# Performance work log

Hardware: AMD Instinct MI355X
Metric: run time of the kernel (lower is better)

## Reference

```python
import jax, jax.numpy as jnp
import numpy as np

B, S, D = 2, 2048, 2048
H = 16
Q_LORA, KV_LORA = 1536, 512
D_NOPE, D_ROPE, D_V = 128, 64, 128
D_QK = D_NOPE + D_ROPE  # 192
EPS = 1e-6


def rmsnorm(x, w):
    return x * jax.lax.rsqrt(jnp.mean(x * x, axis=-1, keepdims=True) + EPS) * w


def apply_rope(x, freqs_cis):
    # x: (B, S, h, D_ROPE); freqs_cis: (S, D_ROPE//2, 2) = (cos, sin)
    # DeepSeek pairs consecutive elements (2i, 2i+1) as complex re/im.
    b, s, h, d = x.shape
    xp = x.reshape(b, s, h, d // 2, 2)
    re, im = xp[..., 0], xp[..., 1]
    cos = freqs_cis[None, :, None, :, 0]
    sin = freqs_cis[None, :, None, :, 1]
    out_re = re * cos - im * sin
    out_im = re * sin + im * cos
    return jnp.stack([out_re, out_im], axis=-1).reshape(b, s, h, d)


def setup_inputs() -> dict:
    key = jax.random.key(0)
    ks = jax.random.split(key, 8)
    sd = 0.02
    x = jax.random.normal(ks[0], (B, S, D), dtype=jnp.float32)
    # RoPE table over the rope head dim
    inv_freq = 1.0 / (10000.0 ** (np.arange(0, D_ROPE, 2, dtype=np.float32) / D_ROPE))
    t = np.arange(S, dtype=np.float32)
    f = np.outer(t, inv_freq)  # (S, 32)
    freqs_cis = jnp.asarray(np.stack([np.cos(f), np.sin(f)], axis=-1), dtype=jnp.float32)
    return {
        "x": x,
        "start_pos": 0,
        "freqs_cis": freqs_cis,
        "wq_a": jax.random.normal(ks[1], (Q_LORA, D), dtype=jnp.float32) * sd,
        "q_norm_w": jnp.ones((Q_LORA,), dtype=jnp.float32),
        "wq_b": jax.random.normal(ks[2], (H * D_QK, Q_LORA), dtype=jnp.float32) * sd,
        "wkv_a": jax.random.normal(ks[3], (KV_LORA + D_ROPE, D), dtype=jnp.float32) * sd,
        "kv_norm_w": jnp.ones((KV_LORA,), dtype=jnp.float32),
        "wkv_b": jax.random.normal(ks[4], (H * (D_NOPE + D_V), KV_LORA), dtype=jnp.float32) * sd,
        "wo": jax.random.normal(ks[5], (D, H * D_V), dtype=jnp.float32) * sd,
    }


def reference(x, start_pos, freqs_cis, wq_a, q_norm_w, wq_b, wkv_a, kv_norm_w, wkv_b, wo):
    bsz, seqlen, _ = x.shape
    softmax_scale = D_QK ** (-0.5)

    # --- queries: low-rank down-proj, RMSNorm, up-proj ---
    q = rmsnorm(x @ wq_a.T, q_norm_w) @ wq_b.T          # (B,S,H*D_QK)
    q = q.reshape(bsz, seqlen, H, D_QK)
    q_nope, q_pe = q[..., :D_NOPE], q[..., D_NOPE:]
    q_pe = apply_rope(q_pe, freqs_cis)
    q = jnp.concatenate([q_nope, q_pe], axis=-1)         # (B,S,H,192)

    # --- keys/values: compressed latent + shared rope key ---
    kv = x @ wkv_a.T                                     # (B,S,KV_LORA+D_ROPE)
    kv_c, k_pe = kv[..., :KV_LORA], kv[..., KV_LORA:]
    k_pe = apply_rope(k_pe[:, :, None, :], freqs_cis)    # (B,S,1,64)
    kvb = rmsnorm(kv_c, kv_norm_w) @ wkv_b.T             # (B,S,H*(D_NOPE+D_V))
    kvb = kvb.reshape(bsz, seqlen, H, D_NOPE + D_V)
    k_nope, v = kvb[..., :D_NOPE], kvb[..., D_NOPE:]
    k = jnp.concatenate([k_nope, jnp.broadcast_to(k_pe, (bsz, seqlen, H, D_ROPE))], axis=-1)

    # --- causal attention (FA2 with attention_mask=None) ---
    scores = jnp.einsum("bqhd,bkhd->bhqk", q, k) * softmax_scale
    causal = jnp.tril(jnp.ones((seqlen, seqlen), dtype=bool))
    scores = jnp.where(causal[None, None], scores, jnp.finfo(scores.dtype).min)
    attn = jax.nn.softmax(scores, axis=-1)
    out = jnp.einsum("bhqk,bkhd->bqhd", attn, v)         # (B,S,H,D_V)
    # (v padding to qk_head_dim then slicing [..., :D_V] is a no-op)
    return out.reshape(bsz, seqlen, H * D_V) @ wo.T
```

## Files before the change

### kernel.cpp

```cpp
#include <hip/hip_runtime.h>
#include <math.h>

typedef short short8 __attribute__((ext_vector_type(8)));
typedef float float4v __attribute__((ext_vector_type(4)));
#define AS1 __attribute__((address_space(1)))
#define AS3 __attribute__((address_space(3)))

__device__ __forceinline__ float b2f(ushort u) {
    unsigned v = ((unsigned)u) << 16; float f; __builtin_memcpy(&f, &v, 4); return f;
}
__device__ __forceinline__ ushort f2b(float f) {
    unsigned v; __builtin_memcpy(&v, &f, 4);
    unsigned r = (v + 0x7fffu + ((v >> 16) & 1u)) >> 16;
    return (ushort)r;
}

__global__ void cvt_pad(const float* __restrict__ src, ushort* __restrict__ dst,
                        int src_rows, int cols, int total4) {
    int i = blockIdx.x * 256 + threadIdx.x;
    if (i >= total4) return;
    size_t e = (size_t)i * 4;
    int r = (int)(e / (size_t)cols);
    ushort4 o;
    if (r < src_rows) {
        float4 v = *(const float4*)(src + e);
        o.x = f2b(v.x); o.y = f2b(v.y); o.z = f2b(v.z); o.w = f2b(v.w);
    } else {
        o.x = 0; o.y = 0; o.z = 0; o.w = 0;
    }
    *(ushort4*)(dst + e) = o;
}

__global__ __launch_bounds__(256)
void gemm_bt(const ushort* __restrict__ A, const ushort* __restrict__ B,
             void* __restrict__ Cv, int K, int lda, int ldb, int ldc, int mode,
             ushort* __restrict__ Kf, ushort* __restrict__ Vtp) {
    __shared__ ushort sA[128 * 32];
    __shared__ ushort sB[128 * 32];
    const int tid = threadIdx.x;
    const int wave = tid >> 6, lane = tid & 63;
    const int bm = blockIdx.y * 128, bn = blockIdx.x * 128;
    const int wm = (wave >> 1) * 64, wn = (wave & 1) * 64;
    const int lq = lane & 15, quad = lane >> 4;
    float4v acc[4][4] = {};

    const int srow = wave * 32 + (lane >> 2);
    const int skc = (lane & 3) * 8;
    const ushort* Ag = A + (size_t)(bm + srow) * lda + skc;
    const ushort* Bg = B + (size_t)(bn + srow) * ldb + skc;
    ushort* sAw = sA + (wave * 32) * 32;
    ushort* sBw = sB + (wave * 32) * 32;

    for (int k0 = 0; k0 < K; k0 += 32) {
        __builtin_amdgcn_global_load_lds((const AS1 void*)(Ag + k0), (AS3 void*)sAw, 16, 0, 0);
        __builtin_amdgcn_global_load_lds((const AS1 void*)(Ag + (size_t)16 * lda + k0),
                                         (AS3 void*)(sAw + 16 * 32), 16, 0, 0);
        __builtin_amdgcn_global_load_lds((const AS1 void*)(Bg + k0), (AS3 void*)sBw, 16, 0, 0);
        __builtin_amdgcn_global_load_lds((const AS1 void*)(Bg + (size_t)16 * ldb + k0),
                                         (AS3 void*)(sBw + 16 * 32), 16, 0, 0);
        __syncthreads();
        short8 af[4], bfr[4];
#pragma unroll
        for (int i = 0; i < 4; ++i) {
            af[i]  = *(const short8*)(sA + (wm + i * 16 + lq) * 32 + quad * 8);
            bfr[i] = *(const short8*)(sB + (wn + i * 16 + lq) * 32 + quad * 8);
        }
#pragma unroll
        for (int i = 0; i < 4; ++i)
#pragma unroll
            for (int j = 0; j < 4; ++j)
                acc[i][j] = __builtin_amdgcn_mfma_f32_16x16x32_bf16(af[i], bfr[j], acc[i][j], 0, 0, 0);
        __syncthreads();
    }
#pragma unroll
    for (int i = 0; i < 4; ++i) {
        int row0 = bm + wm + i * 16 + quad * 4;
#pragma unroll
        for (int j = 0; j < 4; ++j) {
            int col = bn + wn + j * 16 + lq;
            if (mode == 0) {
                ushort* C = (ushort*)Cv;
#pragma unroll
                for (int r = 0; r < 4; ++r)
                    C[(size_t)(row0 + r) * ldc + col] = f2b(acc[i][j][r]);
            } else if (mode == 1) {
                float* C = (float*)Cv;
#pragma unroll
                for (int r = 0; r < 4; ++r)
                    C[(size_t)(row0 + r) * ldc + col] = acc[i][j][r];
            } else {
                int h = col >> 8, c = col & 255;
                int bh = ((row0 >> 11) << 4) + h;
                if (c < 128) {
#pragma unroll
                    for (int r = 0; r < 4; ++r) {
                        int s = (row0 + r) & 2047;
                        Kf[((size_t)bh * 2048 + s) * 200 + c] = f2b(acc[i][j][r]);
                    }
                } else {
                    int d = c - 128;
                    int kt = (row0 & 2047) >> 6, kv = row0 & 63;
                    ushort4 o;
                    o.x = f2b(acc[i][j][0]); o.y = f2b(acc[i][j][1]);
                    o.z = f2b(acc[i][j][2]); o.w = f2b(acc[i][j][3]);
                    *(ushort4*)(Vtp + (((size_t)bh * 32 + kt) * 128 + d) * 72 + kv) = o;
                }
            }
        }
    }
}

__global__ void rmsnorm_inplace(ushort* __restrict__ d, const float* __restrict__ w,
                                int cols, int ld) {
    int row = blockIdx.x, tid = threadIdx.x;
    ushort* p = d + (size_t)row * ld;
    float ss = 0.f;
    for (int i = tid; i < cols; i += 256) { float v = b2f(p[i]); ss += v * v; }
#pragma unroll
    for (int off = 32; off >= 1; off >>= 1) ss += __shfl_xor(ss, off);
    __shared__ float red[4];
    if ((tid & 63) == 0) red[tid >> 6] = ss;
    __syncthreads();
    float tot = red[0] + red[1] + red[2] + red[3];
    float rs = rsqrtf(tot / (float)cols + 1e-6f);
    for (int i = tid; i < cols; i += 256) p[i] = f2b(b2f(p[i]) * rs * w[i]);
}

__global__ void kvnorm_rope(const ushort* __restrict__ kvraw, const float* __restrict__ w,
                            const float* __restrict__ freqs, ushort* __restrict__ kvc,
                            ushort* __restrict__ kpe, int ld) {
    int row = blockIdx.x, tid = threadIdx.x;
    int s = row & 2047;
    const ushort* p = kvraw + (size_t)row * ld;
    float v0 = b2f(p[tid]), v1 = b2f(p[tid + 256]);
    float ss = v0 * v0 + v1 * v1;
#pragma unroll
    for (int off = 32; off >= 1; off >>= 1) ss += __shfl_xor(ss, off);
    __shared__ float red[4];
    if ((tid & 63) == 0) red[tid >> 6] = ss;
    __syncthreads();
    float tot = red[0] + red[1] + red[2] + red[3];
    float rs = rsqrtf(tot / 512.f + 1e-6f);
    kvc[(size_t)row * 512 + tid] = f2b(v0 * rs * w[tid]);
    kvc[(size_t)row * 512 + tid + 256] = f2b(v1 * rs * w[tid + 256]);
    if (tid < 32) {
        float re = b2f(p[512 + 2 * tid]), im = b2f(p[512 + 2 * tid + 1]);
        float cs = freqs[(s * 32 + tid) * 2], sn = freqs[(s * 32 + tid) * 2 + 1];
        kpe[(size_t)row * 64 + 2 * tid] = f2b(re * cs - im * sn);
        kpe[(size_t)row * 64 + 2 * tid + 1] = f2b(re * sn + im * cs);
    }
}

__global__ void qrope(ushort* __restrict__ q, const float* __restrict__ freqs) {
    int idx = blockIdx.x * 256 + threadIdx.x;
    int i = idx & 31;
    int h = (idx >> 5) & 15;
    int srow = idx >> 9;
    int s = srow & 2047;
    ushort* p = q + ((size_t)srow * 16 + h) * 192 + 128 + 2 * i;
    float re = b2f(p[0]), im = b2f(p[1]);
    float cs = freqs[(s * 32 + i) * 2], sn = freqs[(s * 32 + i) * 2 + 1];
    p[0] = f2b(re * cs - im * sn);
    p[1] = f2b(re * sn + im * cs);
}

__global__ void kpe_fill(const ushort* __restrict__ kpe, ushort* __restrict__ Kfull) {
    int tid = threadIdx.x;
    int row = blockIdx.x * 8 + (tid >> 5);
    int c = tid & 31;
    int bh = row >> 11, s = row & 2047, b = bh >> 4;
    ushort2 v;
    v.x = kpe[((size_t)b * 2048 + s) * 64 + 2 * c];
    v.y = kpe[((size_t)b * 2048 + s) * 64 + 2 * c + 1];
    *(ushort2*)(Kfull + (size_t)row * 200 + 128 + 2 * c) = v;
}

__global__ __launch_bounds__(256)
void mla_attn6(const ushort* __restrict__ q, const ushort* __restrict__ Kfull,
               const ushort* __restrict__ Vt, ushort* __restrict__ out, float scale) {
    __shared__ ushort sK[64 * 200];
    __shared__ ushort sV[128 * 72];
    __shared__ ushort sP[4][16][72];
    const int tid = threadIdx.x, wave = tid >> 6, lane = tid & 63;
    const int lq = lane & 15, quad = lane >> 4;
    const int lin = blockIdx.x;
    const int e = lin & 7, idx = lin >> 3;
    const int qt = 31 - (idx >> 2);
    const int bh = e + 8 * (idx & 3);
    const int b = bh >> 4, h = bh & 15;
    const ushort* Kb = Kfull + (size_t)bh * 2048 * 200;
    const ushort* Vb = Vt + (size_t)bh * 32 * 128 * 72;

    const int qrow = qt * 64 + wave * 16 + lq;
    const ushort* qp = q + ((size_t)(b * 2048 + qrow) * 16 + h) * 192 + quad * 8;
    short8 qf[6];
#pragma unroll
    for (int c = 0; c < 6; ++c) qf[c] = *(const short8*)(qp + c * 32);

    float4v oacc[8] = {};
    float m_i[4] = {-INFINITY, -INFINITY, -INFINITY, -INFINITY};
    float l_i[4] = {0.f, 0.f, 0.f, 0.f};
    const int myrow0 = qt * 64 + wave * 16 + quad * 4;

    for (int kt = 0; kt <= qt; ++kt) {
        const ushort* Ksrc = Kb + (size_t)kt * 64 * 200;
        const ushort* Vsrc = Vb + (size_t)kt * 128 * 72;
#pragma unroll
        for (int i = 0; i < 7; ++i) {
            int s0 = i * 256 + wave * 64;
            if (s0 < 1600)
                __builtin_amdgcn_global_load_lds((const AS1 void*)(Ksrc + (size_t)(s0 + lane) * 8),
                                                 (AS3 void*)(sK + s0 * 8), 16, 0, 0);
        }
#pragma unroll
        for (int i = 0; i < 5; ++i) {
            int s0 = i * 256 + wave * 64;
            if (s0 < 1152)
                __builtin_amdgcn_global_load_lds((const AS1 void*)(Vsrc + (size_t)(s0 + lane) * 8),
                                                 (AS3 void*)(sV + s0 * 8), 16, 0, 0);
        }
        __syncthreads();
        float4v sc[4];
#pragma unroll
        for (int ct = 0; ct < 4; ++ct) {
            float4v a = {0.f, 0.f, 0.f, 0.f};
#pragma unroll
            for (int c = 0; c < 6; ++c) {
                short8 kf = *(const short8*)(sK + (ct * 16 + lq) * 200 + c * 32 + quad * 8);
                a = __builtin_amdgcn_mfma_f32_16x16x32_bf16(qf[c], kf, a, 0, 0, 0);
            }
            sc[ct] = a;
        }
        float mnew[4];
#pragma unroll
        for (int r = 0; r < 4; ++r) mnew[r] = m_i[r];
#pragma unroll
        for (int ct = 0; ct < 4; ++ct)
#pragma unroll
            for (int r = 0; r < 4; ++r) {
                float v = sc[ct][r] * scale;
                if (kt == qt && (kt * 64 + ct * 16 + lq) > (myrow0 + r)) v = -INFINITY;
                sc[ct][r] = v;
                mnew[r] = fmaxf(mnew[r], v);
            }
#pragma unroll
        for (int off = 8; off >= 1; off >>= 1)
#pragma unroll
            for (int r = 0; r < 4; ++r) mnew[r] = fmaxf(mnew[r], __shfl_xor(mnew[r], off));
        float alpha[4], psum[4];
#pragma unroll
        for (int r = 0; r < 4; ++r) {
            alpha[r] = __expf(m_i[r] - mnew[r]);
            m_i[r] = mnew[r];
            psum[r] = 0.f;
        }
#pragma unroll
        for (int ct = 0; ct < 4; ++ct)
#pragma unroll
            for (int r = 0; r < 4; ++r) {
                float pv = __expf(sc[ct][r] - mnew[r]);
                psum[r] += pv;
                sP[wave][quad * 4 + r][ct * 16 + lq] = f2b(pv);
            }
#pragma unroll
        for (int off = 8; off >= 1; off >>= 1)
#pragma unroll
            for (int r = 0; r < 4; ++r) psum[r] += __shfl_xor(psum[r], off);
#pragma unroll
        for (int r = 0; r < 4; ++r) l_i[r] = l_i[r] * alpha[r] + psum[r];
#pragma unroll
        for (int dt = 0; dt < 8; ++dt)
#pragma unroll
            for (int r = 0; r < 4; ++r) oacc[dt][r] *= alpha[r];
#pragma unroll
        for (int kc = 0; kc < 2; ++kc) {
            short8 pf = *(const short8*)(&sP[wave][lq][kc * 32 + quad * 8]);
#pragma unroll
            for (int dt = 0; dt < 8; ++dt) {
                short8 vf = *(const short8*)(sV + (dt * 16 + lq) * 72 + kc * 32 + quad * 8);
                oacc[dt] = __builtin_amdgcn_mfma_f32_16x16x32_bf16(pf, vf, oacc[dt], 0, 0, 0);
            }
        }
        __syncthreads();
    }
    float inv[4];
#pragma unroll
    for (int r = 0; r < 4; ++r) inv[r] = 1.f / l_i[r];
#pragma unroll
    for (int dt = 0; dt < 8; ++dt) {
#pragma unroll
        for (int r = 0; r < 4; ++r) {
            out[((size_t)(b * 2048 + myrow0 + r) * 16 + h) * 128 + dt * 16 + lq] =
                f2b(oacc[dt][r] * inv[r]);
        }
    }
}

extern "C" void kernel_launch(void* const* d_in, const int* in_sizes, int n_in,
                              void* d_out, int out_size, void* d_ws, size_t ws_size,
                              hipStream_t stream) {
    const float* x     = (const float*)d_in[0];
    const float* freqs = (const float*)d_in[2];
    const float* wq_a  = (const float*)d_in[3];
    const float* qnw   = (const float*)d_in[4];
    const float* wq_b  = (const float*)d_in[5];
    const float* wkv_a = (const float*)d_in[6];
    const float* kvnw  = (const float*)d_in[7];
    const float* wkv_b = (const float*)d_in[8];
    const float* wo    = (const float*)d_in[9];

    char* ws = (char*)d_ws;
    size_t off = 0;
    auto alloc = [&](size_t n) { char* p = ws + off; off += (n + 255) & ~(size_t)255; return p; };
    ushort* xb    = (ushort*)alloc(4096ull * 2048 * 2);
    ushort* wqkva = (ushort*)alloc(2176ull * 2048 * 2);
    ushort* wqbb  = (ushort*)alloc(3072ull * 1536 * 2);
    ushort* wkvbb = (ushort*)alloc(4096ull * 512 * 2);
    ushort* wob   = (ushort*)alloc(2048ull * 2048 * 2);
    ushort* qakv  = (ushort*)alloc(4096ull * 2176 * 2);
    ushort* kvc   = (ushort*)alloc(4096ull * 512 * 2);
    ushort* kpe   = (ushort*)alloc(4096ull * 64 * 2);
    ushort* qfull = (ushort*)alloc(4096ull * 3072 * 2);
    ushort* kvbuf = (ushort*)alloc(4096ull * 4096 * 2);
    ushort* attno = (ushort*)alloc(4096ull * 2048 * 2);
    if (off > ws_size) return;
    ushort* Kfull = kvbuf;
    ushort* Vt = xb;

    auto cvt = [&](const float* s, ushort* dd, int sr, int cols, size_t dtot) {
        int t4 = (int)(dtot / 4);
        cvt_pad<<<(t4 + 255) / 256, 256, 0, stream>>>(s, dd, sr, cols, t4);
    };
    cvt(x, xb, 4096, 2048, 4096ull * 2048);
    cvt(wq_a, wqkva, 1536, 2048, 1536ull * 2048);
    cvt(wkv_a, wqkva + 1536ull * 2048, 576, 2048, 640ull * 2048);
    cvt(wq_b, wqbb, 3072, 1536, 3072ull * 1536);
    cvt(wkv_b, wkvbb, 4096, 512, 4096ull * 512);
    cvt(wo, wob, 2048, 2048, 2048ull * 2048);

    gemm_bt<<<dim3(17, 32), 256, 0, stream>>>(xb, wqkva, qakv, 2048, 2048, 2048, 2176, 0, nullptr, nullptr);
    rmsnorm_inplace<<<4096, 256, 0, stream>>>(qakv, qnw, 1536, 2176);
    kvnorm_rope<<<4096, 256, 0, stream>>>(qakv + 1536, kvnw, freqs, kvc, kpe, 2176);
    gemm_bt<<<dim3(24, 32), 256, 0, stream>>>(qakv, wqbb, qfull, 1536, 2176, 1536, 3072, 0, nullptr, nullptr);
    qrope<<<8192, 256, 0, stream>>>(qfull, freqs);
    kpe_fill<<<8192, 256, 0, stream>>>(kpe, Kfull);
    gemm_bt<<<dim3(32, 32), 256, 0, stream>>>(kvc, wkvbb, nullptr, 512, 512, 512, 0, 2, Kfull, Vt);
    const float scale = 1.0f / sqrtf(192.0f);
    mla_attn6<<<dim3(1024), 256, 0, stream>>>(qfull, Kfull, Vt, attno, scale);
    gemm_bt<<<dim3(16, 32), 256, 0, stream>>>(attno, wob, (float*)d_out, 2048, 2048, 2048, 2048, 1, nullptr, nullptr);
}
```

Baseline: 511.8 us.

## Register-prefetch next K/V tile, fold softmax scale into wq_b, lazy rescale

The attention kernel now loads the next K/V tile into registers while the current tile is being computed, then writes it to LDS at the top of the next iteration. Previously it used direct global-to-LDS loads with no overlap. The softmax scale and log2(e) are folded into the bf16 conversion of wq_b so the kernel can use exp2 without a per-score multiply. The running-max rescale of the output accumulator is skipped unless some row's max grows by more than 8. These changes add register pressure, with launch bounds set to 3 blocks per CU, and the lazy rescale slightly alters numerics.

```diff
diff --git a/kernel.cpp b/kernel.cpp
--- a/kernel.cpp
+++ b/kernel.cpp
@@ -16,7 +16,7 @@
 }
 
 __global__ void cvt_pad(const float* __restrict__ src, ushort* __restrict__ dst,
-                        int src_rows, int cols, int total4) {
+                        int src_rows, int cols, int total4, float scl) {
     int i = blockIdx.x * 256 + threadIdx.x;
     if (i >= total4) return;
     size_t e = (size_t)i * 4;
@@ -24,7 +24,7 @@
     ushort4 o;
     if (r < src_rows) {
         float4 v = *(const float4*)(src + e);
-        o.x = f2b(v.x); o.y = f2b(v.y); o.z = f2b(v.z); o.w = f2b(v.w);
+        o.x = f2b(v.x * scl); o.y = f2b(v.y * scl); o.z = f2b(v.z * scl); o.w = f2b(v.w * scl);
     } else {
         o.x = 0; o.y = 0; o.z = 0; o.w = 0;
     }
@@ -175,9 +175,9 @@
     *(ushort2*)(Kfull + (size_t)row * 200 + 128 + 2 * c) = v;
 }
 
-__global__ __launch_bounds__(256)
-void mla_attn6(const ushort* __restrict__ q, const ushort* __restrict__ Kfull,
-               const ushort* __restrict__ Vt, ushort* __restrict__ out, float scale) {
+__global__ __launch_bounds__(256, 3)
+void mla_attn7(const ushort* __restrict__ q, const ushort* __restrict__ Kfull,
+               const ushort* __restrict__ Vt, ushort* __restrict__ out) {
     __shared__ ushort sK[64 * 200];
     __shared__ ushort sV[128 * 72];
     __shared__ ushort sP[4][16][72];
@@ -190,12 +190,25 @@
     const int b = bh >> 4, h = bh & 15;
     const ushort* Kb = Kfull + (size_t)bh * 2048 * 200;
     const ushort* Vb = Vt + (size_t)bh * 32 * 128 * 72;
+    const int slot = wave * 64 + lane;
 
     const int qrow = qt * 64 + wave * 16 + lq;
     const ushort* qp = q + ((size_t)(b * 2048 + qrow) * 16 + h) * 192 + quad * 8;
     short8 qf[6];
 #pragma unroll
     for (int c = 0; c < 6; ++c) qf[c] = *(const short8*)(qp + c * 32);
+
+    short8 kreg[7], vreg[5];
+#pragma unroll
+    for (int i = 0; i < 7; ++i) {
+        int s0 = i * 256 + slot;
+        if (s0 < 1600) kreg[i] = *(const short8*)(Kb + (size_t)s0 * 8);
+    }
+#pragma unroll
+    for (int i = 0; i < 5; ++i) {
+        int s0 = i * 256 + slot;
+        if (s0 < 1152) vreg[i] = *(const short8*)(Vb + (size_t)s0 * 8);
+    }
 
     float4v oacc[8] = {};
     float m_i[4] = {-INFINITY, -INFINITY, -INFINITY, -INFINITY};
@@ -203,23 +216,31 @@
     const int myrow0 = qt * 64 + wave * 16 + quad * 4;
 
     for (int kt = 0; kt <= qt; ++kt) {
-        const ushort* Ksrc = Kb + (size_t)kt * 64 * 200;
-        const ushort* Vsrc = Vb + (size_t)kt * 128 * 72;
 #pragma unroll
         for (int i = 0; i < 7; ++i) {
-            int s0 = i * 256 + wave * 64;
-            if (s0 < 1600)
-                __builtin_amdgcn_global_load_lds((const AS1 void*)(Ksrc + (size_t)(s0 + lane) * 8),
-                                                 (AS3 void*)(sK + s0 * 8), 16, 0, 0);
+            int s0 = i * 256 + slot;
+            if (s0 < 1600) *(short8*)(sK + (size_t)s0 * 8) = kreg[i];
         }
 #pragma unroll
         for (int i = 0; i < 5; ++i) {
-            int s0 = i * 256 + wave * 64;
-            if (s0 < 1152)
-                __builtin_amdgcn_global_load_lds((const AS1 void*)(Vsrc + (size_t)(s0 + lane) * 8),
-                                                 (AS3 void*)(sV + s0 * 8), 16, 0, 0);
+            int s0 = i * 256 + slot;
+            if (s0 < 1152) *(short8*)(sV + (size_t)s0 * 8) = vreg[i];
         }
         __syncthreads();
+        if (kt < qt) {
+            const ushort* Ksrc = Kb + (size_t)(kt + 1) * 64 * 200;
+            const ushort* Vsrc = Vb + (size_t)(kt + 1) * 128 * 72;
+#pragma unroll
+            for (int i = 0; i < 7; ++i) {
+                int s0 = i * 256 + slot;
+                if (s0 < 1600) kreg[i] = *(const short8*)(Ksrc + (size_t)s0 * 8);
+            }
+#pragma unroll
+            for (int i = 0; i < 5; ++i) {
+                int s0 = i * 256 + slot;
+                if (s0 < 1152) vreg[i] = *(const short8*)(Vsrc + (size_t)s0 * 8);
+            }
+        }
         float4v sc[4];
 #pragma unroll
         for (int ct = 0; ct < 4; ++ct) {
@@ -238,7 +259,7 @@
         for (int ct = 0; ct < 4; ++ct)
 #pragma unroll
             for (int r = 0; r < 4; ++r) {
-                float v = sc[ct][r] * scale;
+                float v = sc[ct][r];
                 if (kt == qt && (kt * 64 + ct * 16 + lq) > (myrow0 + r)) v = -INFINITY;
                 sc[ct][r] = v;
                 mnew[r] = fmaxf(mnew[r], v);
@@ -247,18 +268,25 @@
         for (int off = 8; off >= 1; off >>= 1)
 #pragma unroll
             for (int r = 0; r < 4; ++r) mnew[r] = fmaxf(mnew[r], __shfl_xor(mnew[r], off));
-        float alpha[4], psum[4];
-#pragma unroll
-        for (int r = 0; r < 4; ++r) {
-            alpha[r] = __expf(m_i[r] - mnew[r]);
-            m_i[r] = mnew[r];
-            psum[r] = 0.f;
-        }
+        float g = mnew[0] - m_i[0];
+#pragma unroll
+        for (int r = 1; r < 4; ++r) g = fmaxf(g, mnew[r] - m_i[r]);
+        if (__ballot(g > 8.0f) != 0ull) {
+#pragma unroll
+            for (int r = 0; r < 4; ++r) {
+                float a = __builtin_amdgcn_exp2f(m_i[r] - mnew[r]);
+                m_i[r] = mnew[r];
+                l_i[r] *= a;
+#pragma unroll
+                for (int dt = 0; dt < 8; ++dt) oacc[dt][r] *= a;
+            }
+        }
+        float psum[4] = {0.f, 0.f, 0.f, 0.f};
 #pragma unroll
         for (int ct = 0; ct < 4; ++ct)
 #pragma unroll
             for (int r = 0; r < 4; ++r) {
-                float pv = __expf(sc[ct][r] - mnew[r]);
+                float pv = __builtin_amdgcn_exp2f(sc[ct][r] - m_i[r]);
                 psum[r] += pv;
                 sP[wave][quad * 4 + r][ct * 16 + lq] = f2b(pv);
             }
@@ -267,11 +295,7 @@
 #pragma unroll
             for (int r = 0; r < 4; ++r) psum[r] += __shfl_xor(psum[r], off);
 #pragma unroll
-        for (int r = 0; r < 4; ++r) l_i[r] = l_i[r] * alpha[r] + psum[r];
-#pragma unroll
-        for (int dt = 0; dt < 8; ++dt)
-#pragma unroll
-            for (int r = 0; r < 4; ++r) oacc[dt][r] *= alpha[r];
+        for (int r = 0; r < 4; ++r) l_i[r] += psum[r];
 #pragma unroll
         for (int kc = 0; kc < 2; ++kc) {
             short8 pf = *(const short8*)(&sP[wave][lq][kc * 32 + quad * 8]);
@@ -327,16 +351,17 @@
     ushort* Kfull = kvbuf;
     ushort* Vt = xb;
 
-    auto cvt = [&](const float* s, ushort* dd, int sr, int cols, size_t dtot) {
+    auto cvt = [&](const float* s, ushort* dd, int sr, int cols, size_t dtot, float scl) {
         int t4 = (int)(dtot / 4);
-        cvt_pad<<<(t4 + 255) / 256, 256, 0, stream>>>(s, dd, sr, cols, t4);
+        cvt_pad<<<(t4 + 255) / 256, 256, 0, stream>>>(s, dd, sr, cols, t4, scl);
     };
-    cvt(x, xb, 4096, 2048, 4096ull * 2048);
-    cvt(wq_a, wqkva, 1536, 2048, 1536ull * 2048);
-    cvt(wkv_a, wqkva + 1536ull * 2048, 576, 2048, 640ull * 2048);
-    cvt(wq_b, wqbb, 3072, 1536, 3072ull * 1536);
-    cvt(wkv_b, wkvbb, 4096, 512, 4096ull * 512);
-    cvt(wo, wob, 2048, 2048, 2048ull * 2048);
+    const float qk_scale = 1.44269504f / sqrtf(192.0f);
+    cvt(x, xb, 4096, 2048, 4096ull * 2048, 1.f);
+    cvt(wq_a, wqkva, 1536, 2048, 1536ull * 2048, 1.f);
+    cvt(wkv_a, wqkva + 1536ull * 2048, 576, 2048, 640ull * 2048, 1.f);
+    cvt(wq_b, wqbb, 3072, 1536, 3072ull * 1536, qk_scale);
+    cvt(wkv_b, wkvbb, 4096, 512, 4096ull * 512, 1.f);
+    cvt(wo, wob, 2048, 2048, 2048ull * 2048, 1.f);
 
     gemm_bt<<<dim3(17, 32), 256, 0, stream>>>(xb, wqkva, qakv, 2048, 2048, 2048, 2176, 0, nullptr, nullptr);
     rmsnorm_inplace<<<4096, 256, 0, stream>>>(qakv, qnw, 1536, 2176);
@@ -345,7 +370,6 @@
     qrope<<<8192, 256, 0, stream>>>(qfull, freqs);
     kpe_fill<<<8192, 256, 0, stream>>>(kpe, Kfull);
     gemm_bt<<<dim3(32, 32), 256, 0, stream>>>(kvc, wkvbb, nullptr, 512, 512, 512, 0, 2, Kfull, Vt);
-    const float scale = 1.0f / sqrtf(192.0f);
-    mla_attn6<<<dim3(1024), 256, 0, stream>>>(qfull, Kfull, Vt, attno, scale);
+    mla_attn7<<<dim3(1024), 256, 0, stream>>>(qfull, Kfull, Vt, attno);
     gemm_bt<<<dim3(16, 32), 256, 0, stream>>>(attno, wob, (float*)d_out, 2048, 2048, 2048, 2048, 1, nullptr, nullptr);
 }
```

Measured after the change: 509.7 us. Within noise of the previous version (-0.4%).
